# Optimization experiments

Measured on AMD Instinct MI355X. Metric: run time of the kernel, lower is better.

## Reference

```python
import jax, jax.numpy as jnp
import numpy as np

C_Z = 128
H = 4
D = C_Z // H          # head_dim = 32
BASE = 2 * D // 2     # base_feature_dim = feature_map_multiplier*head_dim//2 = 32
BSZ, S = 1, 256
EPS_LN = 1e-5


def _lin_params(key, fan_in, fan_out):
    kw, kb = jax.random.split(key)
    bound = 1.0 / np.sqrt(fan_in)
    w = jax.random.uniform(kw, (fan_out, fan_in), jnp.float32, -bound, bound)
    b = jax.random.uniform(kb, (fan_out,), jnp.float32, -bound, bound)
    return w, b


def setup_inputs() -> dict:
    key = jax.random.key(0)
    ks = jax.random.split(key, 9)
    z = jax.random.normal(ks[0], (BSZ, S, S, C_Z), jnp.float32)
    pair_mask = jax.random.randint(ks[1], (BSZ, S, S), 0, 2, jnp.int32)
    q_w, q_b = _lin_params(ks[2], C_Z, C_Z)
    k_w, k_b = _lin_params(ks[3], C_Z, C_Z)
    v_w, v_b = _lin_params(ks[4], C_Z, C_Z)
    qf_w, qf_b = _lin_params(ks[5], D, BASE)
    kf_w, kf_b = _lin_params(ks[6], D, BASE)
    g_w, g_b = _lin_params(ks[7], C_Z, C_Z)
    o_w, o_b = _lin_params(ks[8], C_Z, C_Z)
    return {
        'z': z, 'pair_mask': pair_mask,
        'ln_w': jnp.ones((C_Z,), jnp.float32), 'ln_b': jnp.zeros((C_Z,), jnp.float32),
        'q_w': q_w, 'q_b': q_b, 'k_w': k_w, 'k_b': k_b, 'v_w': v_w, 'v_b': v_b,
        'qf_w': qf_w, 'qf_b': qf_b, 'kf_w': kf_w, 'kf_b': kf_b,
        'g_w': g_w, 'g_b': g_b, 'o_w': o_w, 'o_b': o_b,
    }


def _feature_map(t, w, b):
    m = jnp.clip(t @ w.T + b, -8.0, 8.0)
    return jnp.concatenate([jnp.exp(m), jnp.exp(-m)], axis=-1)


def reference(z, pair_mask, ln_w, ln_b, q_w, q_b, k_w, k_b, v_w, v_b,
              qf_w, qf_b, kf_w, kf_b, g_w, g_b, o_w, o_b):
    bsz, seq, _, c = z.shape
    h, d = H, c // H
    mask = pair_mask.astype(z.dtype)                         # [B,S,S]

    # LayerNorm over last dim
    mu = jnp.mean(z, axis=-1, keepdims=True)
    var = jnp.mean(jnp.square(z - mu), axis=-1, keepdims=True)
    zn = (z - mu) * jax.lax.rsqrt(var + EPS_LN) * ln_w + ln_b

    z_rows = zn.reshape(bsz * seq, seq, c)                   # [BS, N, C]
    row_mask = mask.reshape(bsz * seq, seq)[:, None, :, None]  # [BS,1,N,1]

    def proj(w, b):
        return (z_rows @ w.T + b).reshape(bsz * seq, seq, h, d).transpose(0, 2, 1, 3)

    q = proj(q_w, q_b)                                       # [BS,H,N,D]
    k = proj(k_w, k_b)
    v = proj(v_w, v_b) * row_mask

    qf = _feature_map(q, qf_w, qf_b)                         # [BS,H,N,F]
    kf = _feature_map(k, kf_w, kf_b) * row_mask

    kv = jnp.einsum('bhnd,bhne->bhde', kf, v)                # [BS,H,F,D]
    k_sum = kf.sum(axis=-2)                                  # [BS,H,F]
    denom = jnp.maximum(jnp.einsum('bhnd,bhd->bhn', qf, k_sum), 1e-6)
    out = jnp.einsum('bhnd,bhde->bhne', qf, kv) / denom[..., None]

    out = out.transpose(0, 2, 1, 3).reshape(bsz * seq, seq, c)
    gate = jax.nn.sigmoid(z_rows @ g_w.T + g_b)
    out = (gate * out) @ o_w.T + o_b
    out = out.reshape(bsz, seq, seq, c)
    return out * mask[..., None]
```

## Files before the change

kernel.cpp:

```cpp
#include <hip/hip_runtime.h>
#include <stdint.h>

#define DEV __device__ __forceinline__

typedef unsigned short u16;
typedef unsigned int u32;
typedef short bh8 __attribute__((ext_vector_type(8)));
typedef float f32x4 __attribute__((ext_vector_type(4)));

DEV float bf2f(u16 v){ return __uint_as_float(((u32)v)<<16); }
DEV u16 f2bf(float f){
    u32 x = __float_as_uint(f);
    x += 0x7fffu + ((x>>16)&1u);
    return (u16)(x>>16);
}
DEV void cvt8(int4 r, float* f){
    u32 a=(u32)r.x, b=(u32)r.y, c=(u32)r.z, d=(u32)r.w;
    f[0]=__uint_as_float(a<<16); f[1]=__uint_as_float(a&0xffff0000u);
    f[2]=__uint_as_float(b<<16); f[3]=__uint_as_float(b&0xffff0000u);
    f[4]=__uint_as_float(c<<16); f[5]=__uint_as_float(c&0xffff0000u);
    f[6]=__uint_as_float(d<<16); f[7]=__uint_as_float(d&0xffff0000u);
}
DEV bh8 ld_frag(const u16* p){
    int4 v = *(const int4*)p;
    union{ int4 i; bh8 h; } u; u.i = v; return u.h;
}
#define MFMA __builtin_amdgcn_mfma_f32_16x16x32_bf16


#define P_LNW 0
#define P_LNB 128
#define P_QW  256
#define P_QB  16640
#define P_KW  16768
#define P_KB  33152
#define P_VW  33280
#define P_VB  49664
#define P_QFW 49792
#define P_QFB 50816
#define P_KFW 50848
#define P_KFB 51872
#define P_GW  51904
#define P_GB  68288
#define P_OW  68416
#define P_OB  84800
#define P_TOT 84928
#define P_CQW 84928
#define P_CQB 101312
#define P_CKW 101440
#define P_CKB 117824
#define P_XTOT 117952

__global__ void detect_kernel(const u32* __restrict__ z, u32* __restrict__ flag){
    int tid = threadIdx.x;
    u32 w = z[(size_t)tid*997];
    u32 b0 = w & 0xFFFFu;
    int e = (int)((b0>>7)&0xFF);
    int good = (e>=96 && e<=150) ? 1 : 0;
    __shared__ int red[4];
    #pragma unroll
    for(int o=1;o<64;o<<=1) good += __shfl_xor(good,o,64);
    if((tid&63)==0) red[tid>>6]=good;
    __syncthreads();
    if(tid==0) *flag = ((red[0]+red[1]+red[2]+red[3]) > 192) ? 1u : 0u;
}

__global__ void convert_params(
    const void* p0, const void* p1, const void* p2, const void* p3,
    const void* p4, const void* p5, const void* p6, const void* p7,
    const void* p8, const void* p9, const void* p10, const void* p11,
    const void* p12, const void* p13, const void* p14, const void* p15,
    const u32* __restrict__ flag, u16* __restrict__ dst){
    int idx = blockIdx.x*256 + threadIdx.x;
    if(idx >= P_TOT) return;
    const int offs[17] = {P_LNW,P_LNB,P_QW,P_QB,P_KW,P_KB,P_VW,P_VB,
                          P_QFW,P_QFB,P_KFW,P_KFB,P_GW,P_GB,P_OW,P_OB,P_TOT};
    const void* ptrs[16] = {p0,p1,p2,p3,p4,p5,p6,p7,p8,p9,p10,p11,p12,p13,p14,p15};
    int tsel = 0;
    #pragma unroll
    for(int i=1;i<16;++i) if(idx >= offs[i]) tsel = i;
    int local = idx - offs[tsel];
    u16 v;
    if(*flag) v = ((const u16*)ptrs[tsel])[local];
    else      v = f2bf(((const float*)ptrs[tsel])[local]);
    dst[idx] = v;
}

__global__ void prep_combine(u16* __restrict__ pb){
    if(blockIdx.x < 128){
        int idx = blockIdx.x*256 + threadIdx.x;
        int sel = idx >> 14;
        int rem = idx & 16383;
        int h = rem >> 12, j = (rem >> 7) & 31, c = rem & 127;
        int FW = sel ? P_KFW : P_QFW;
        int W  = sel ? P_KW  : P_QW;
        float s = 0.f;
        #pragma unroll
        for(int d=0; d<32; ++d)
            s += bf2f(pb[FW + j*32 + d]) * bf2f(pb[W + (h*32+d)*128 + c]);
        pb[(sel ? P_CKW : P_CQW) + h*4096 + j*128 + c] = f2bf(s);
    } else {
        int t = threadIdx.x;
        int sel = t >> 7, h = (t >> 5) & 3, j = t & 31;
        int FW = sel ? P_KFW : P_QFW;
        int FB = sel ? P_KFB : P_QFB;
        int B  = sel ? P_KB  : P_QB;
        float s = bf2f(pb[FB + j]);
        #pragma unroll
        for(int d=0; d<32; ++d)
            s += bf2f(pb[FW + j*32 + d]) * bf2f(pb[B + h*32 + d]);
        pb[(sel ? P_CKB : P_CQB) + h*32 + j] = f2bf(s);
    }
}

__global__ void ln_kernel(const void* __restrict__ zv, const u16* __restrict__ pb,
                          const u32* __restrict__ flag, u16* __restrict__ zn){
    int t = blockIdx.x*4 + (threadIdx.x>>6);
    int lane = threadIdx.x & 63;
    float x0, x1;
    if(*flag){
        u32 pr = ((const u32*)zv)[(size_t)t*64 + lane];
        x0 = __uint_as_float(pr<<16); x1 = __uint_as_float(pr & 0xffff0000u);
    } else {
        float2 v = ((const float2*)zv)[(size_t)t*64 + lane];
        x0 = v.x; x1 = v.y;
    }
    float s = x0 + x1, s2 = x0*x0 + x1*x1;
    #pragma unroll
    for(int o=1;o<64;o<<=1){ s += __shfl_xor(s,o,64); s2 += __shfl_xor(s2,o,64); }
    float mean = s*(1.f/128.f);
    float var  = s2*(1.f/128.f) - mean*mean;
    float rs = rsqrtf(var + 1e-5f);
    int c0 = 2*lane;
    float w0 = bf2f(pb[P_LNW+c0]), w1 = bf2f(pb[P_LNW+c0+1]);
    float b0 = bf2f(pb[P_LNB+c0]), b1 = bf2f(pb[P_LNB+c0+1]);
    float o0 = (x0-mean)*rs*w0 + b0;
    float o1 = (x1-mean)*rs*w1 + b1;
    u32 po = (u32)f2bf(o0) | ((u32)f2bf(o1)<<16);
    *(u32*)(zn + (size_t)t*128 + c0) = po;
}

#define ST_N 264
#define ST_F 68
#define SM_KF   1024
#define SM_VT   34816
#define SM_QF   1024
#define SM_KVT  52240
#define SM_TOT  56736

__global__ __launch_bounds__(256,1)
void mega_kernel(const u16* __restrict__ zn, const int* __restrict__ mask,
                 const u16* __restrict__ pb, u16* __restrict__ attn){
    __shared__ __align__(16) char smem[SM_TOT];
    float* mask_f = (float*)smem;
    u16* kfT = (u16*)(smem + SM_KF);
    u16* vT  = (u16*)(smem + SM_VT);
    u16* qf  = (u16*)(smem + SM_QF);
    u16* kvT = (u16*)(smem + SM_KVT);

    int row = blockIdx.x;
    int tid = threadIdx.x, lane = tid & 63, wv = tid >> 6;
    int lm = lane & 15, quad = lane >> 4;

    mask_f[tid] = (float)mask[row*256 + tid];
    if(tid < 64){
        int2 ones; ones.x = 0x3F803F80; ones.y = 0x3F803F80;
        *(int2*)(vT + 32*ST_N + tid*4) = ones;
    }

    bh8 a[4][4];
    {
        const u16* Ab = zn + ((size_t)row*256 + wv*64 + lm)*128 + quad*8;
        #pragma unroll
        for(int mt=0; mt<4; ++mt)
            #pragma unroll
            for(int ks=0; ks<4; ++ks)
                a[mt][ks] = ld_frag(Ab + (size_t)mt*16*128 + ks*32);
    }
    bh8 onesf;
    { union{int4 i; bh8 h;} u; u.i.x=u.i.y=u.i.z=u.i.w=0x3F803F80; onesf = u.h; }

    __syncthreads();

    for(int h=0; h<4; ++h){
        f32x4 gacc[4][2];
        {
            f32x4 acc[4][2];
            #pragma unroll
            for(int mt=0;mt<4;++mt){ acc[mt][0]=(f32x4){0,0,0,0}; acc[mt][1]=(f32x4){0,0,0,0}; }
            #pragma unroll
            for(int ks=0; ks<4; ++ks){
                bh8 b0 = ld_frag(pb + P_CKW + h*4096 + lm*128      + ks*32 + quad*8);
                bh8 b1 = ld_frag(pb + P_CKW + h*4096 + (16+lm)*128 + ks*32 + quad*8);
                #pragma unroll
                for(int mt=0; mt<4; ++mt){
                    acc[mt][0] = MFMA(a[mt][ks], b0, acc[mt][0], 0,0,0);
                    acc[mt][1] = MFMA(a[mt][ks], b1, acc[mt][1], 0,0,0);
                }
            }
            float bb0 = bf2f(pb[P_CKB + h*32 + lm]);
            float bb1 = bf2f(pb[P_CKB + h*32 + 16 + lm]);
            #pragma unroll
            for(int mt=0; mt<4; ++mt)
                #pragma unroll
                for(int r=0; r<4; ++r){
                    int n = wv*64 + mt*16 + quad*4 + r;
                    float mk = mask_f[n];
                    float m0 = fminf(8.f, fmaxf(-8.f, acc[mt][0][r] + bb0));
                    float m1 = fminf(8.f, fmaxf(-8.f, acc[mt][1][r] + bb1));
                    kfT[(lm   )*ST_N + n] = f2bf(__expf( m0)*mk);
                    kfT[(lm+32)*ST_N + n] = f2bf(__expf(-m0)*mk);
                    kfT[(lm+16)*ST_N + n] = f2bf(__expf( m1)*mk);
                    kfT[(lm+48)*ST_N + n] = f2bf(__expf(-m1)*mk);
                }
        }
        {
            f32x4 acc[4][2];
            #pragma unroll
            for(int mt=0;mt<4;++mt){ acc[mt][0]=(f32x4){0,0,0,0}; acc[mt][1]=(f32x4){0,0,0,0}; }
            #pragma unroll
            for(int ks=0; ks<4; ++ks){
                bh8 b0 = ld_frag(pb + P_VW + (size_t)(h*32 + lm)*128      + ks*32 + quad*8);
                bh8 b1 = ld_frag(pb + P_VW + (size_t)(h*32 + 16 + lm)*128 + ks*32 + quad*8);
                #pragma unroll
                for(int mt=0; mt<4; ++mt){
                    acc[mt][0] = MFMA(a[mt][ks], b0, acc[mt][0], 0,0,0);
                    acc[mt][1] = MFMA(a[mt][ks], b1, acc[mt][1], 0,0,0);
                }
            }
            float bb0 = bf2f(pb[P_VB + h*32 + lm]);
            float bb1 = bf2f(pb[P_VB + h*32 + 16 + lm]);
            #pragma unroll
            for(int mt=0; mt<4; ++mt)
                #pragma unroll
                for(int r=0; r<4; ++r){
                    int n = wv*64 + mt*16 + quad*4 + r;
                    float mk = mask_f[n];
                    vT[(lm   )*ST_N + n] = f2bf((acc[mt][0][r] + bb0)*mk);
                    vT[(16+lm)*ST_N + n] = f2bf((acc[mt][1][r] + bb1)*mk);
                }
        }
        {
            f32x4 acc[4][2];
            #pragma unroll
            for(int mt=0;mt<4;++mt){ acc[mt][0]=(f32x4){0,0,0,0}; acc[mt][1]=(f32x4){0,0,0,0}; }
            #pragma unroll
            for(int ks=0; ks<4; ++ks){
                bh8 b0 = ld_frag(pb + P_GW + (size_t)(h*32 + lm)*128      + ks*32 + quad*8);
                bh8 b1 = ld_frag(pb + P_GW + (size_t)(h*32 + 16 + lm)*128 + ks*32 + quad*8);
                #pragma unroll
                for(int mt=0; mt<4; ++mt){
                    acc[mt][0] = MFMA(a[mt][ks], b0, acc[mt][0], 0,0,0);
                    acc[mt][1] = MFMA(a[mt][ks], b1, acc[mt][1], 0,0,0);
                }
            }
            float bb0 = bf2f(pb[P_GB + h*32 + lm]);
            float bb1 = bf2f(pb[P_GB + h*32 + 16 + lm]);
            #pragma unroll
            for(int mt=0; mt<4; ++mt)
                #pragma unroll
                for(int r=0; r<4; ++r){
                    gacc[mt][0][r] = 1.f/(1.f + __expf(-(acc[mt][0][r] + bb0)));
                    gacc[mt][1][r] = 1.f/(1.f + __expf(-(acc[mt][1][r] + bb1)));
                }
        }
        __syncthreads();
        {
            f32x4 acc0=(f32x4){0,0,0,0}, acc1=(f32x4){0,0,0,0}, acc2=(f32x4){0,0,0,0};
            #pragma unroll
            for(int ks=0; ks<8; ++ks){
                bh8 aa = ld_frag(kfT + (size_t)(wv*16+lm)*ST_N + ks*32 + quad*8);
                bh8 b0 = ld_frag(vT + (size_t)lm*ST_N      + ks*32 + quad*8);
                bh8 b1 = ld_frag(vT + (size_t)(16+lm)*ST_N + ks*32 + quad*8);
                acc0 = MFMA(aa, b0, acc0, 0,0,0);
                acc1 = MFMA(aa, b1, acc1, 0,0,0);
                acc2 = MFMA(aa, onesf, acc2, 0,0,0);
            }
            #pragma unroll
            for(int r=0; r<4; ++r){
                int f = wv*16 + quad*4 + r;
                kvT[(lm   )*ST_F + f] = f2bf(acc0[r]);
                kvT[(16+lm)*ST_F + f] = f2bf(acc1[r]);
                if(lm==0) kvT[32*ST_F + f] = f2bf(acc2[r]);
            }
        }
        __syncthreads();
        {
            f32x4 acc[4][2];
            #pragma unroll
            for(int mt=0;mt<4;++mt){ acc[mt][0]=(f32x4){0,0,0,0}; acc[mt][1]=(f32x4){0,0,0,0}; }
            #pragma unroll
            for(int ks=0; ks<4; ++ks){
                bh8 b0 = ld_frag(pb + P_CQW + h*4096 + lm*128      + ks*32 + quad*8);
                bh8 b1 = ld_frag(pb + P_CQW + h*4096 + (16+lm)*128 + ks*32 + quad*8);
                #pragma unroll
                for(int mt=0; mt<4; ++mt){
                    acc[mt][0] = MFMA(a[mt][ks], b0, acc[mt][0], 0,0,0);
                    acc[mt][1] = MFMA(a[mt][ks], b1, acc[mt][1], 0,0,0);
                }
            }
            float bb0 = bf2f(pb[P_CQB + h*32 + lm]);
            float bb1 = bf2f(pb[P_CQB + h*32 + 16 + lm]);
            #pragma unroll
            for(int mt=0; mt<4; ++mt)
                #pragma unroll
                for(int r=0; r<4; ++r){
                    int n = wv*64 + mt*16 + quad*4 + r;
                    float m0 = fminf(8.f, fmaxf(-8.f, acc[mt][0][r] + bb0));
                    float m1 = fminf(8.f, fmaxf(-8.f, acc[mt][1][r] + bb1));
                    qf[n*ST_F + lm     ] = f2bf(__expf( m0));
                    qf[n*ST_F + lm + 32] = f2bf(__expf(-m0));
                    qf[n*ST_F + lm + 16] = f2bf(__expf( m1));
                    qf[n*ST_F + lm + 48] = f2bf(__expf(-m1));
                }
        }
        __syncthreads();
        {
            f32x4 acc[4][3];
            #pragma unroll
            for(int mt=0;mt<4;++mt)
                #pragma unroll
                for(int nt=0;nt<3;++nt) acc[mt][nt]=(f32x4){0,0,0,0};
            #pragma unroll
            for(int ks=0; ks<2; ++ks){
                bh8 b0 = ld_frag(kvT + (size_t)lm*ST_F      + ks*32 + quad*8);
                bh8 b1 = ld_frag(kvT + (size_t)(16+lm)*ST_F + ks*32 + quad*8);
                bh8 b2 = ld_frag(kvT + (size_t)32*ST_F      + ks*32 + quad*8);
                #pragma unroll
                for(int mt=0; mt<4; ++mt){
                    bh8 aa = ld_frag(qf + (size_t)(wv*64+mt*16+lm)*ST_F + ks*32 + quad*8);
                    acc[mt][0] = MFMA(aa, b0, acc[mt][0], 0,0,0);
                    acc[mt][1] = MFMA(aa, b1, acc[mt][1], 0,0,0);
                    acc[mt][2] = MFMA(aa, b2, acc[mt][2], 0,0,0);
                }
            }
            #pragma unroll
            for(int mt=0; mt<4; ++mt)
                #pragma unroll
                for(int r=0; r<4; ++r){
                    int n = wv*64 + mt*16 + quad*4 + r;
                    float den = acc[mt][2][r];
                    float rcp = 1.f / fmaxf(den, 1e-6f);
                    u16* op = attn + ((size_t)row*256 + n)*128 + h*32;
                    op[lm]      = f2bf(acc[mt][0][r]*rcp*gacc[mt][0][r]);
                    op[16+lm]   = f2bf(acc[mt][1][r]*rcp*gacc[mt][1][r]);
                }
        }
        __syncthreads();
    }
}

#define LDS_P 136
__global__ __launch_bounds__(256,2)
void oproj_kernel(const u16* __restrict__ attn, const u16* __restrict__ pb,
                  const int* __restrict__ mask, const u32* __restrict__ flagp,
                  void* __restrict__ out){
    __shared__ u16 st[128*LDS_P];
    int tid = threadIdx.x;
    int lane = tid&63, wv = tid>>6;
    int mhalf = (wv>>1)*64, nhalf = (wv&1)*64;
    int lm = lane&15, quad = lane>>4;
    int m0 = blockIdx.x*128;

    f32x4 acc[4][4];
    #pragma unroll
    for(int mt=0;mt<4;++mt)
        #pragma unroll
        for(int nt=0;nt<4;++nt)
            acc[mt][nt] = (f32x4){0.f,0.f,0.f,0.f};

    const u16* Abase = attn + (size_t)(m0 + mhalf + lm)*128 + quad*8;
    const u16* W = pb + P_OW;
    #pragma unroll
    for(int ks=0; ks<4; ++ks){
        bh8 a[4], b[4];
        #pragma unroll
        for(int mt=0; mt<4; ++mt)
            a[mt] = ld_frag(Abase + (size_t)mt*16*128 + ks*32);
        #pragma unroll
        for(int nt=0; nt<4; ++nt)
            b[nt] = ld_frag(W + (size_t)(nhalf + nt*16 + lm)*128 + ks*32 + quad*8);
        #pragma unroll
        for(int mt=0; mt<4; ++mt)
            #pragma unroll
            for(int nt=0; nt<4; ++nt)
                acc[mt][nt] = MFMA(a[mt], b[nt], acc[mt][nt], 0, 0, 0);
    }
    float bv[4];
    #pragma unroll
    for(int nt=0; nt<4; ++nt) bv[nt] = bf2f(pb[P_OB + nhalf + nt*16 + lm]);
    #pragma unroll
    for(int mt=0; mt<4; ++mt){
        int mrow = m0 + mhalf + mt*16 + quad*4;
        float mk[4];
        #pragma unroll
        for(int r=0;r<4;++r) mk[r] = (float)mask[mrow+r];
        #pragma unroll
        for(int nt=0; nt<4; ++nt)
            #pragma unroll
            for(int r=0; r<4; ++r){
                float x = (acc[mt][nt][r] + bv[nt]) * mk[r];
                st[(mhalf + mt*16 + quad*4 + r)*LDS_P + nhalf + nt*16 + lm] = f2bf(x);
            }
    }
    __syncthreads();
    {
        int row = tid>>1, half = tid&1;
        const u16* src = st + row*LDS_P + half*64;
        bool isbf = (*flagp != 0u);
        if(isbf){
            u16* dst = (u16*)out + (size_t)(m0 + row)*128 + half*64;
            #pragma unroll
            for(int it=0; it<8; ++it)
                ((int4*)dst)[it] = ((const int4*)src)[it];
        } else {
            float* dst = (float*)out + (size_t)(m0 + row)*128 + half*64;
            #pragma unroll
            for(int it=0; it<8; ++it){
                float f[8]; cvt8(((const int4*)src)[it], f);
                float4 lo; lo.x=f[0]; lo.y=f[1]; lo.z=f[2]; lo.w=f[3];
                float4 hi; hi.x=f[4]; hi.y=f[5]; hi.z=f[6]; hi.w=f[7];
                ((float4*)dst)[it*2  ] = lo;
                ((float4*)dst)[it*2+1] = hi;
            }
        }
    }
}

extern "C" void kernel_launch(void* const* d_in, const int* in_sizes, int n_in,
                              void* d_out, int out_size, void* d_ws, size_t ws_size,
                              hipStream_t stream){
    const void* z    = d_in[0];
    const int*  mask = (const int*)d_in[1];

    char* ws = (char*)d_ws;
    const size_t MB = (size_t)1<<20;
    u16*   zn   = (u16*)(ws + 0*MB);
    u16*   attn = (u16*)(ws + 16*MB);
    u16*   pb   = (u16*)(ws + 32*MB);
    u32*   flag = (u32*)(ws + 33*MB);

    detect_kernel<<<1,256,0,stream>>>((const u32*)z, flag);
    convert_params<<<(P_TOT+255)/256,256,0,stream>>>(
        d_in[2], d_in[3], d_in[4], d_in[5], d_in[6], d_in[7], d_in[8], d_in[9],
        d_in[10], d_in[11], d_in[12], d_in[13], d_in[14], d_in[15], d_in[16], d_in[17],
        flag, pb);
    prep_combine<<<129,256,0,stream>>>(pb);
    ln_kernel<<<16384,256,0,stream>>>(z, pb, flag, zn);
    mega_kernel<<<256,256,0,stream>>>(zn, mask, pb, attn);
    oproj_kernel<<<512,256,0,stream>>>(attn, pb, mask, flag, d_out);
}
```

Before: 188.9 us.

## Split attention mega-kernel per head and fuse parameter prep kernels

The attention kernel now launches one block per (row, head) pair instead of looping over four heads inside one block per row, and allows two blocks per CU. The goal is more parallel blocks and latency hiding on a GPU that previously had only one 4-wave block per row. In exchange, each row's normalized activations are loaded from memory four times, once per head block. Separately, the parameter conversion and combined-weight precompute kernels are merged into a single launch that reads raw inputs directly, and several LDS scatter stores are packed into 8-byte writes.

```diff
diff --git a/kernel.cpp b/kernel.cpp
--- a/kernel.cpp
+++ b/kernel.cpp
@@ -21,9 +21,18 @@
     f[4]=__uint_as_float(c<<16); f[5]=__uint_as_float(c&0xffff0000u);
     f[6]=__uint_as_float(d<<16); f[7]=__uint_as_float(d&0xffff0000u);
 }
+DEV int2 pk4(float a, float b, float c, float d){
+    int2 r;
+    r.x = (int)((u32)f2bf(a) | ((u32)f2bf(b)<<16));
+    r.y = (int)((u32)f2bf(c) | ((u32)f2bf(d)<<16));
+    return r;
+}
 DEV bh8 ld_frag(const u16* p){
     int4 v = *(const int4*)p;
     union{ int4 i; bh8 h; } u; u.i = v; return u.h;
+}
+DEV float ldp(const void* p, int i, bool bf){
+    return bf ? bf2f(((const u16*)p)[i]) : ((const float*)p)[i];
 }
 #define MFMA __builtin_amdgcn_mfma_f32_16x16x32_bf16
 
@@ -49,7 +58,8 @@
 #define P_CQB 101312
 #define P_CKW 101440
 #define P_CKB 117824
-#define P_XTOT 117952
+
+#define NCONV 332
 
 __global__ void detect_kernel(const u32* __restrict__ z, u32* __restrict__ flag){
     int tid = threadIdx.x;
@@ -65,51 +75,48 @@
     if(tid==0) *flag = ((red[0]+red[1]+red[2]+red[3]) > 192) ? 1u : 0u;
 }
 
-__global__ void convert_params(
+__global__ void prep_params(
     const void* p0, const void* p1, const void* p2, const void* p3,
     const void* p4, const void* p5, const void* p6, const void* p7,
     const void* p8, const void* p9, const void* p10, const void* p11,
     const void* p12, const void* p13, const void* p14, const void* p15,
     const u32* __restrict__ flag, u16* __restrict__ dst){
-    int idx = blockIdx.x*256 + threadIdx.x;
-    if(idx >= P_TOT) return;
-    const int offs[17] = {P_LNW,P_LNB,P_QW,P_QB,P_KW,P_KB,P_VW,P_VB,
-                          P_QFW,P_QFB,P_KFW,P_KFB,P_GW,P_GB,P_OW,P_OB,P_TOT};
-    const void* ptrs[16] = {p0,p1,p2,p3,p4,p5,p6,p7,p8,p9,p10,p11,p12,p13,p14,p15};
-    int tsel = 0;
-    #pragma unroll
-    for(int i=1;i<16;++i) if(idx >= offs[i]) tsel = i;
-    int local = idx - offs[tsel];
-    u16 v;
-    if(*flag) v = ((const u16*)ptrs[tsel])[local];
-    else      v = f2bf(((const float*)ptrs[tsel])[local]);
-    dst[idx] = v;
-}
-
-__global__ void prep_combine(u16* __restrict__ pb){
-    if(blockIdx.x < 128){
-        int idx = blockIdx.x*256 + threadIdx.x;
+    bool bf = (*flag != 0u);
+    int b = blockIdx.x, tid = threadIdx.x;
+    if(b < NCONV){
+        int idx = b*256 + tid;
+        if(idx >= P_TOT) return;
+        const int offs[17] = {P_LNW,P_LNB,P_QW,P_QB,P_KW,P_KB,P_VW,P_VB,
+                              P_QFW,P_QFB,P_KFW,P_KFB,P_GW,P_GB,P_OW,P_OB,P_TOT};
+        const void* ptrs[16] = {p0,p1,p2,p3,p4,p5,p6,p7,p8,p9,p10,p11,p12,p13,p14,p15};
+        int tsel = 0;
+        #pragma unroll
+        for(int i=1;i<16;++i) if(idx >= offs[i]) tsel = i;
+        dst[idx] = bf ? ((const u16*)ptrs[tsel])[idx - offs[tsel]]
+                      : f2bf(((const float*)ptrs[tsel])[idx - offs[tsel]]);
+    } else if(b < NCONV + 128){
+        int idx = (b - NCONV)*256 + tid;
         int sel = idx >> 14;
         int rem = idx & 16383;
         int h = rem >> 12, j = (rem >> 7) & 31, c = rem & 127;
-        int FW = sel ? P_KFW : P_QFW;
-        int W  = sel ? P_KW  : P_QW;
+        const void* FWp = sel ? p10 : p8;
+        const void* Wp  = sel ? p4  : p2;
         float s = 0.f;
         #pragma unroll
         for(int d=0; d<32; ++d)
-            s += bf2f(pb[FW + j*32 + d]) * bf2f(pb[W + (h*32+d)*128 + c]);
-        pb[(sel ? P_CKW : P_CQW) + h*4096 + j*128 + c] = f2bf(s);
+            s += ldp(FWp, j*32+d, bf) * ldp(Wp, (h*32+d)*128 + c, bf);
+        dst[(sel ? P_CKW : P_CQW) + h*4096 + j*128 + c] = f2bf(s);
     } else {
-        int t = threadIdx.x;
+        int t = tid;
         int sel = t >> 7, h = (t >> 5) & 3, j = t & 31;
-        int FW = sel ? P_KFW : P_QFW;
-        int FB = sel ? P_KFB : P_QFB;
-        int B  = sel ? P_KB  : P_QB;
-        float s = bf2f(pb[FB + j]);
+        const void* FWp = sel ? p10 : p8;
+        const void* FBp = sel ? p11 : p9;
+        const void* Bp  = sel ? p5  : p3;
+        float s = ldp(FBp, j, bf);
         #pragma unroll
         for(int d=0; d<32; ++d)
-            s += bf2f(pb[FW + j*32 + d]) * bf2f(pb[B + h*32 + d]);
-        pb[(sel ? P_CKB : P_CQB) + h*32 + j] = f2bf(s);
+            s += ldp(FWp, j*32+d, bf) * ldp(Bp, h*32+d, bf);
+        dst[(sel ? P_CKB : P_CQB) + h*32 + j] = f2bf(s);
     }
 }
 
@@ -145,10 +152,10 @@
 #define SM_KF   1024
 #define SM_VT   34816
 #define SM_QF   1024
-#define SM_KVT  52240
-#define SM_TOT  56736
-
-__global__ __launch_bounds__(256,1)
+#define SM_KVT  51712
+#define SM_TOT  56200
+
+__global__ __launch_bounds__(256,2)
 void mega_kernel(const u16* __restrict__ zn, const int* __restrict__ mask,
                  const u16* __restrict__ pb, u16* __restrict__ attn){
     __shared__ __align__(16) char smem[SM_TOT];
@@ -158,15 +165,11 @@
     u16* qf  = (u16*)(smem + SM_QF);
     u16* kvT = (u16*)(smem + SM_KVT);
 
-    int row = blockIdx.x;
+    int g = blockIdx.x, row = g>>2, h = g&3;
     int tid = threadIdx.x, lane = tid & 63, wv = tid >> 6;
     int lm = lane & 15, quad = lane >> 4;
 
     mask_f[tid] = (float)mask[row*256 + tid];
-    if(tid < 64){
-        int2 ones; ones.x = 0x3F803F80; ones.y = 0x3F803F80;
-        *(int2*)(vT + 32*ST_N + tid*4) = ones;
-    }
 
     bh8 a[4][4];
     {
@@ -182,171 +185,173 @@
 
     __syncthreads();
 
-    for(int h=0; h<4; ++h){
-        f32x4 gacc[4][2];
-        {
-            f32x4 acc[4][2];
-            #pragma unroll
-            for(int mt=0;mt<4;++mt){ acc[mt][0]=(f32x4){0,0,0,0}; acc[mt][1]=(f32x4){0,0,0,0}; }
-            #pragma unroll
-            for(int ks=0; ks<4; ++ks){
-                bh8 b0 = ld_frag(pb + P_CKW + h*4096 + lm*128      + ks*32 + quad*8);
-                bh8 b1 = ld_frag(pb + P_CKW + h*4096 + (16+lm)*128 + ks*32 + quad*8);
-                #pragma unroll
-                for(int mt=0; mt<4; ++mt){
-                    acc[mt][0] = MFMA(a[mt][ks], b0, acc[mt][0], 0,0,0);
-                    acc[mt][1] = MFMA(a[mt][ks], b1, acc[mt][1], 0,0,0);
-                }
-            }
-            float bb0 = bf2f(pb[P_CKB + h*32 + lm]);
-            float bb1 = bf2f(pb[P_CKB + h*32 + 16 + lm]);
-            #pragma unroll
-            for(int mt=0; mt<4; ++mt)
-                #pragma unroll
-                for(int r=0; r<4; ++r){
-                    int n = wv*64 + mt*16 + quad*4 + r;
-                    float mk = mask_f[n];
-                    float m0 = fminf(8.f, fmaxf(-8.f, acc[mt][0][r] + bb0));
-                    float m1 = fminf(8.f, fmaxf(-8.f, acc[mt][1][r] + bb1));
-                    kfT[(lm   )*ST_N + n] = f2bf(__expf( m0)*mk);
-                    kfT[(lm+32)*ST_N + n] = f2bf(__expf(-m0)*mk);
-                    kfT[(lm+16)*ST_N + n] = f2bf(__expf( m1)*mk);
-                    kfT[(lm+48)*ST_N + n] = f2bf(__expf(-m1)*mk);
-                }
-        }
-        {
-            f32x4 acc[4][2];
-            #pragma unroll
-            for(int mt=0;mt<4;++mt){ acc[mt][0]=(f32x4){0,0,0,0}; acc[mt][1]=(f32x4){0,0,0,0}; }
-            #pragma unroll
-            for(int ks=0; ks<4; ++ks){
-                bh8 b0 = ld_frag(pb + P_VW + (size_t)(h*32 + lm)*128      + ks*32 + quad*8);
-                bh8 b1 = ld_frag(pb + P_VW + (size_t)(h*32 + 16 + lm)*128 + ks*32 + quad*8);
-                #pragma unroll
-                for(int mt=0; mt<4; ++mt){
-                    acc[mt][0] = MFMA(a[mt][ks], b0, acc[mt][0], 0,0,0);
-                    acc[mt][1] = MFMA(a[mt][ks], b1, acc[mt][1], 0,0,0);
-                }
-            }
-            float bb0 = bf2f(pb[P_VB + h*32 + lm]);
-            float bb1 = bf2f(pb[P_VB + h*32 + 16 + lm]);
-            #pragma unroll
-            for(int mt=0; mt<4; ++mt)
-                #pragma unroll
-                for(int r=0; r<4; ++r){
-                    int n = wv*64 + mt*16 + quad*4 + r;
-                    float mk = mask_f[n];
-                    vT[(lm   )*ST_N + n] = f2bf((acc[mt][0][r] + bb0)*mk);
-                    vT[(16+lm)*ST_N + n] = f2bf((acc[mt][1][r] + bb1)*mk);
-                }
-        }
-        {
-            f32x4 acc[4][2];
-            #pragma unroll
-            for(int mt=0;mt<4;++mt){ acc[mt][0]=(f32x4){0,0,0,0}; acc[mt][1]=(f32x4){0,0,0,0}; }
-            #pragma unroll
-            for(int ks=0; ks<4; ++ks){
-                bh8 b0 = ld_frag(pb + P_GW + (size_t)(h*32 + lm)*128      + ks*32 + quad*8);
-                bh8 b1 = ld_frag(pb + P_GW + (size_t)(h*32 + 16 + lm)*128 + ks*32 + quad*8);
-                #pragma unroll
-                for(int mt=0; mt<4; ++mt){
-                    acc[mt][0] = MFMA(a[mt][ks], b0, acc[mt][0], 0,0,0);
-                    acc[mt][1] = MFMA(a[mt][ks], b1, acc[mt][1], 0,0,0);
-                }
-            }
-            float bb0 = bf2f(pb[P_GB + h*32 + lm]);
-            float bb1 = bf2f(pb[P_GB + h*32 + 16 + lm]);
-            #pragma unroll
-            for(int mt=0; mt<4; ++mt)
-                #pragma unroll
-                for(int r=0; r<4; ++r){
-                    gacc[mt][0][r] = 1.f/(1.f + __expf(-(acc[mt][0][r] + bb0)));
-                    gacc[mt][1][r] = 1.f/(1.f + __expf(-(acc[mt][1][r] + bb1)));
-                }
-        }
-        __syncthreads();
-        {
-            f32x4 acc0=(f32x4){0,0,0,0}, acc1=(f32x4){0,0,0,0}, acc2=(f32x4){0,0,0,0};
-            #pragma unroll
-            for(int ks=0; ks<8; ++ks){
-                bh8 aa = ld_frag(kfT + (size_t)(wv*16+lm)*ST_N + ks*32 + quad*8);
-                bh8 b0 = ld_frag(vT + (size_t)lm*ST_N      + ks*32 + quad*8);
-                bh8 b1 = ld_frag(vT + (size_t)(16+lm)*ST_N + ks*32 + quad*8);
-                acc0 = MFMA(aa, b0, acc0, 0,0,0);
-                acc1 = MFMA(aa, b1, acc1, 0,0,0);
-                acc2 = MFMA(aa, onesf, acc2, 0,0,0);
-            }
-            #pragma unroll
-            for(int r=0; r<4; ++r){
-                int f = wv*16 + quad*4 + r;
-                kvT[(lm   )*ST_F + f] = f2bf(acc0[r]);
-                kvT[(16+lm)*ST_F + f] = f2bf(acc1[r]);
-                if(lm==0) kvT[32*ST_F + f] = f2bf(acc2[r]);
-            }
-        }
-        __syncthreads();
-        {
-            f32x4 acc[4][2];
-            #pragma unroll
-            for(int mt=0;mt<4;++mt){ acc[mt][0]=(f32x4){0,0,0,0}; acc[mt][1]=(f32x4){0,0,0,0}; }
-            #pragma unroll
-            for(int ks=0; ks<4; ++ks){
-                bh8 b0 = ld_frag(pb + P_CQW + h*4096 + lm*128      + ks*32 + quad*8);
-                bh8 b1 = ld_frag(pb + P_CQW + h*4096 + (16+lm)*128 + ks*32 + quad*8);
-                #pragma unroll
-                for(int mt=0; mt<4; ++mt){
-                    acc[mt][0] = MFMA(a[mt][ks], b0, acc[mt][0], 0,0,0);
-                    acc[mt][1] = MFMA(a[mt][ks], b1, acc[mt][1], 0,0,0);
-                }
-            }
-            float bb0 = bf2f(pb[P_CQB + h*32 + lm]);
-            float bb1 = bf2f(pb[P_CQB + h*32 + 16 + lm]);
-            #pragma unroll
-            for(int mt=0; mt<4; ++mt)
-                #pragma unroll
-                for(int r=0; r<4; ++r){
-                    int n = wv*64 + mt*16 + quad*4 + r;
-                    float m0 = fminf(8.f, fmaxf(-8.f, acc[mt][0][r] + bb0));
-                    float m1 = fminf(8.f, fmaxf(-8.f, acc[mt][1][r] + bb1));
-                    qf[n*ST_F + lm     ] = f2bf(__expf( m0));
-                    qf[n*ST_F + lm + 32] = f2bf(__expf(-m0));
-                    qf[n*ST_F + lm + 16] = f2bf(__expf( m1));
-                    qf[n*ST_F + lm + 48] = f2bf(__expf(-m1));
-                }
-        }
-        __syncthreads();
-        {
-            f32x4 acc[4][3];
-            #pragma unroll
-            for(int mt=0;mt<4;++mt)
-                #pragma unroll
-                for(int nt=0;nt<3;++nt) acc[mt][nt]=(f32x4){0,0,0,0};
-            #pragma unroll
-            for(int ks=0; ks<2; ++ks){
-                bh8 b0 = ld_frag(kvT + (size_t)lm*ST_F      + ks*32 + quad*8);
-                bh8 b1 = ld_frag(kvT + (size_t)(16+lm)*ST_F + ks*32 + quad*8);
-                bh8 b2 = ld_frag(kvT + (size_t)32*ST_F      + ks*32 + quad*8);
-                #pragma unroll
-                for(int mt=0; mt<4; ++mt){
-                    bh8 aa = ld_frag(qf + (size_t)(wv*64+mt*16+lm)*ST_F + ks*32 + quad*8);
-                    acc[mt][0] = MFMA(aa, b0, acc[mt][0], 0,0,0);
-                    acc[mt][1] = MFMA(aa, b1, acc[mt][1], 0,0,0);
-                    acc[mt][2] = MFMA(aa, b2, acc[mt][2], 0,0,0);
-                }
-            }
-            #pragma unroll
-            for(int mt=0; mt<4; ++mt)
-                #pragma unroll
-                for(int r=0; r<4; ++r){
-                    int n = wv*64 + mt*16 + quad*4 + r;
-                    float den = acc[mt][2][r];
-                    float rcp = 1.f / fmaxf(den, 1e-6f);
-                    u16* op = attn + ((size_t)row*256 + n)*128 + h*32;
-                    op[lm]      = f2bf(acc[mt][0][r]*rcp*gacc[mt][0][r]);
-                    op[16+lm]   = f2bf(acc[mt][1][r]*rcp*gacc[mt][1][r]);
-                }
-        }
-        __syncthreads();
+    f32x4 gacc[4][2];
+    {
+        f32x4 acc[4][2];
+        #pragma unroll
+        for(int mt=0;mt<4;++mt){ acc[mt][0]=(f32x4){0,0,0,0}; acc[mt][1]=(f32x4){0,0,0,0}; }
+        #pragma unroll
+        for(int ks=0; ks<4; ++ks){
+            bh8 b0 = ld_frag(pb + P_CKW + h*4096 + lm*128      + ks*32 + quad*8);
+            bh8 b1 = ld_frag(pb + P_CKW + h*4096 + (16+lm)*128 + ks*32 + quad*8);
+            #pragma unroll
+            for(int mt=0; mt<4; ++mt){
+                acc[mt][0] = MFMA(a[mt][ks], b0, acc[mt][0], 0,0,0);
+                acc[mt][1] = MFMA(a[mt][ks], b1, acc[mt][1], 0,0,0);
+            }
+        }
+        float bb0 = bf2f(pb[P_CKB + h*32 + lm]);
+        float bb1 = bf2f(pb[P_CKB + h*32 + 16 + lm]);
+        #pragma unroll
+        for(int mt=0; mt<4; ++mt){
+            int n0 = wv*64 + mt*16 + quad*4;
+            float e0p[4], e0m[4], e1p[4], e1m[4];
+            #pragma unroll
+            for(int r=0; r<4; ++r){
+                float mk = mask_f[n0+r];
+                float m0 = fminf(8.f, fmaxf(-8.f, acc[mt][0][r] + bb0));
+                float m1 = fminf(8.f, fmaxf(-8.f, acc[mt][1][r] + bb1));
+                e0p[r] = __expf( m0)*mk;  e0m[r] = __expf(-m0)*mk;
+                e1p[r] = __expf( m1)*mk;  e1m[r] = __expf(-m1)*mk;
+            }
+            *(int2*)(kfT + (size_t)(lm   )*ST_N + n0) = pk4(e0p[0],e0p[1],e0p[2],e0p[3]);
+            *(int2*)(kfT + (size_t)(lm+32)*ST_N + n0) = pk4(e0m[0],e0m[1],e0m[2],e0m[3]);
+            *(int2*)(kfT + (size_t)(lm+16)*ST_N + n0) = pk4(e1p[0],e1p[1],e1p[2],e1p[3]);
+            *(int2*)(kfT + (size_t)(lm+48)*ST_N + n0) = pk4(e1m[0],e1m[1],e1m[2],e1m[3]);
+        }
+    }
+    {
+        f32x4 acc[4][2];
+        #pragma unroll
+        for(int mt=0;mt<4;++mt){ acc[mt][0]=(f32x4){0,0,0,0}; acc[mt][1]=(f32x4){0,0,0,0}; }
+        #pragma unroll
+        for(int ks=0; ks<4; ++ks){
+            bh8 b0 = ld_frag(pb + P_VW + (size_t)(h*32 + lm)*128      + ks*32 + quad*8);
+            bh8 b1 = ld_frag(pb + P_VW + (size_t)(h*32 + 16 + lm)*128 + ks*32 + quad*8);
+            #pragma unroll
+            for(int mt=0; mt<4; ++mt){
+                acc[mt][0] = MFMA(a[mt][ks], b0, acc[mt][0], 0,0,0);
+                acc[mt][1] = MFMA(a[mt][ks], b1, acc[mt][1], 0,0,0);
+            }
+        }
+        float bb0 = bf2f(pb[P_VB + h*32 + lm]);
+        float bb1 = bf2f(pb[P_VB + h*32 + 16 + lm]);
+        #pragma unroll
+        for(int mt=0; mt<4; ++mt){
+            int n0 = wv*64 + mt*16 + quad*4;
+            float v0[4], v1[4];
+            #pragma unroll
+            for(int r=0; r<4; ++r){
+                float mk = mask_f[n0+r];
+                v0[r] = (acc[mt][0][r] + bb0)*mk;
+                v1[r] = (acc[mt][1][r] + bb1)*mk;
+            }
+            *(int2*)(vT + (size_t)(lm   )*ST_N + n0) = pk4(v0[0],v0[1],v0[2],v0[3]);
+            *(int2*)(vT + (size_t)(16+lm)*ST_N + n0) = pk4(v1[0],v1[1],v1[2],v1[3]);
+        }
+    }
+    {
+        f32x4 acc[4][2];
+        #pragma unroll
+        for(int mt=0;mt<4;++mt){ acc[mt][0]=(f32x4){0,0,0,0}; acc[mt][1]=(f32x4){0,0,0,0}; }
+        #pragma unroll
+        for(int ks=0; ks<4; ++ks){
+            bh8 b0 = ld_frag(pb + P_GW + (size_t)(h*32 + lm)*128      + ks*32 + quad*8);
+            bh8 b1 = ld_frag(pb + P_GW + (size_t)(h*32 + 16 + lm)*128 + ks*32 + quad*8);
+            #pragma unroll
+            for(int mt=0; mt<4; ++mt){
+                acc[mt][0] = MFMA(a[mt][ks], b0, acc[mt][0], 0,0,0);
+                acc[mt][1] = MFMA(a[mt][ks], b1, acc[mt][1], 0,0,0);
+            }
+        }
+        float bb0 = bf2f(pb[P_GB + h*32 + lm]);
+        float bb1 = bf2f(pb[P_GB + h*32 + 16 + lm]);
+        #pragma unroll
+        for(int mt=0; mt<4; ++mt)
+            #pragma unroll
+            for(int r=0; r<4; ++r){
+                gacc[mt][0][r] = 1.f/(1.f + __expf(-(acc[mt][0][r] + bb0)));
+                gacc[mt][1][r] = 1.f/(1.f + __expf(-(acc[mt][1][r] + bb1)));
+            }
+    }
+    __syncthreads();
+    {
+        f32x4 acc0=(f32x4){0,0,0,0}, acc1=(f32x4){0,0,0,0}, acc2=(f32x4){0,0,0,0};
+        #pragma unroll
+        for(int ks=0; ks<8; ++ks){
+            bh8 aa = ld_frag(kfT + (size_t)(wv*16+lm)*ST_N + ks*32 + quad*8);
+            bh8 b0 = ld_frag(vT + (size_t)lm*ST_N      + ks*32 + quad*8);
+            bh8 b1 = ld_frag(vT + (size_t)(16+lm)*ST_N + ks*32 + quad*8);
+            acc0 = MFMA(aa, b0, acc0, 0,0,0);
+            acc1 = MFMA(aa, b1, acc1, 0,0,0);
+            acc2 = MFMA(aa, onesf, acc2, 0,0,0);
+        }
+        int f0 = wv*16 + quad*4;
+        *(int2*)(kvT + (size_t)(lm   )*ST_F + f0) = pk4(acc0[0],acc0[1],acc0[2],acc0[3]);
+        *(int2*)(kvT + (size_t)(16+lm)*ST_F + f0) = pk4(acc1[0],acc1[1],acc1[2],acc1[3]);
+        if(lm==0)
+            *(int2*)(kvT + (size_t)32*ST_F + f0) = pk4(acc2[0],acc2[1],acc2[2],acc2[3]);
+    }
+    __syncthreads();
+    {
+        f32x4 acc[4][2];
+        #pragma unroll
+        for(int mt=0;mt<4;++mt){ acc[mt][0]=(f32x4){0,0,0,0}; acc[mt][1]=(f32x4){0,0,0,0}; }
+        #pragma unroll
+        for(int ks=0; ks<4; ++ks){
+            bh8 b0 = ld_frag(pb + P_CQW + h*4096 + lm*128      + ks*32 + quad*8);
+            bh8 b1 = ld_frag(pb + P_CQW + h*4096 + (16+lm)*128 + ks*32 + quad*8);
+            #pragma unroll
+            for(int mt=0; mt<4; ++mt){
+                acc[mt][0] = MFMA(a[mt][ks], b0, acc[mt][0], 0,0,0);
+                acc[mt][1] = MFMA(a[mt][ks], b1, acc[mt][1], 0,0,0);
+            }
+        }
+        float bb0 = bf2f(pb[P_CQB + h*32 + lm]);
+        float bb1 = bf2f(pb[P_CQB + h*32 + 16 + lm]);
+        #pragma unroll
+        for(int mt=0; mt<4; ++mt)
+            #pragma unroll
+            for(int r=0; r<4; ++r){
+                int n = wv*64 + mt*16 + quad*4 + r;
+                float m0 = fminf(8.f, fmaxf(-8.f, acc[mt][0][r] + bb0));
+                float m1 = fminf(8.f, fmaxf(-8.f, acc[mt][1][r] + bb1));
+                qf[n*ST_F + lm     ] = f2bf(__expf( m0));
+                qf[n*ST_F + lm + 32] = f2bf(__expf(-m0));
+                qf[n*ST_F + lm + 16] = f2bf(__expf( m1));
+                qf[n*ST_F + lm + 48] = f2bf(__expf(-m1));
+            }
+    }
+    __syncthreads();
+    {
+        f32x4 acc[4][3];
+        #pragma unroll
+        for(int mt=0;mt<4;++mt)
+            #pragma unroll
+            for(int nt=0;nt<3;++nt) acc[mt][nt]=(f32x4){0,0,0,0};
+        #pragma unroll
+        for(int ks=0; ks<2; ++ks){
+            bh8 b0 = ld_frag(kvT + (size_t)lm*ST_F      + ks*32 + quad*8);
+            bh8 b1 = ld_frag(kvT + (size_t)(16+lm)*ST_F + ks*32 + quad*8);
+            bh8 b2 = ld_frag(kvT + (size_t)32*ST_F      + ks*32 + quad*8);
+            #pragma unroll
+            for(int mt=0; mt<4; ++mt){
+                bh8 aa = ld_frag(qf + (size_t)(wv*64+mt*16+lm)*ST_F + ks*32 + quad*8);
+                acc[mt][0] = MFMA(aa, b0, acc[mt][0], 0,0,0);
+                acc[mt][1] = MFMA(aa, b1, acc[mt][1], 0,0,0);
+                acc[mt][2] = MFMA(aa, b2, acc[mt][2], 0,0,0);
+            }
+        }
+        #pragma unroll
+        for(int mt=0; mt<4; ++mt)
+            #pragma unroll
+            for(int r=0; r<4; ++r){
+                int n = wv*64 + mt*16 + quad*4 + r;
+                float rcp = 1.f / fmaxf(acc[mt][2][r], 1e-6f);
+                u16* op = attn + ((size_t)row*256 + n)*128 + h*32;
+                op[lm]    = f2bf(acc[mt][0][r]*rcp*gacc[mt][0][r]);
+                op[16+lm] = f2bf(acc[mt][1][r]*rcp*gacc[mt][1][r]);
+            }
     }
 }
 
@@ -441,12 +446,11 @@
     u32*   flag = (u32*)(ws + 33*MB);
 
     detect_kernel<<<1,256,0,stream>>>((const u32*)z, flag);
-    convert_params<<<(P_TOT+255)/256,256,0,stream>>>(
+    prep_params<<<NCONV+129,256,0,stream>>>(
         d_in[2], d_in[3], d_in[4], d_in[5], d_in[6], d_in[7], d_in[8], d_in[9],
         d_in[10], d_in[11], d_in[12], d_in[13], d_in[14], d_in[15], d_in[16], d_in[17],
         flag, pb);
-    prep_combine<<<129,256,0,stream>>>(pb);
     ln_kernel<<<16384,256,0,stream>>>(z, pb, flag, zn);
-    mega_kernel<<<256,256,0,stream>>>(zn, mask, pb, attn);
+    mega_kernel<<<1024,256,0,stream>>>(zn, mask, pb, attn);
     oproj_kernel<<<512,256,0,stream>>>(attn, pb, mask, flag, d_out);
 }
```

After: 189.6 us. Within noise of the previous version (+0.4%).
